# Kernel optimization log

Measured on AMD Instinct MI355X. Metric: run time of the kernel, lower is better.

## Reference

```python
import jax, jax.numpy as jnp
import numpy as np

NODE_DIM, HIDDEN_DIM, OUT_DIM = 64, 128, 64
N_NODES, N_EDGES = 50000, 800000
SLOPE = 0.05


def leaky(x):
    return jnp.where(x >= 0, x, SLOPE * x)


def setup_inputs() -> dict:
    key = jax.random.key(0)
    ks = jax.random.split(key, 8)
    x = jax.random.normal(ks[0], (N_NODES, NODE_DIM), dtype=jnp.float32)
    edge_index = jax.random.randint(ks[1], (2, N_EDGES), 0, N_NODES, dtype=jnp.int64)
    s0 = 1.0 / np.sqrt(NODE_DIM)
    s1 = 1.0 / np.sqrt(HIDDEN_DIM)
    W0 = jax.random.uniform(ks[2], (NODE_DIM, HIDDEN_DIM), jnp.float32, -s0, s0)
    b0 = jax.random.uniform(ks[3], (HIDDEN_DIM,), jnp.float32, -s0, s0)
    W1 = jax.random.uniform(ks[4], (HIDDEN_DIM, HIDDEN_DIM), jnp.float32, -s1, s1)
    b1 = jax.random.uniform(ks[5], (HIDDEN_DIM,), jnp.float32, -s1, s1)
    W2 = jax.random.uniform(ks[6], (HIDDEN_DIM, OUT_DIM), jnp.float32, -s1, s1)
    b2 = jax.random.uniform(ks[7], (OUT_DIM,), jnp.float32, -s1, s1)
    return {"x": x, "edge_index": edge_index, "W0": W0, "b0": b0,
            "W1": W1, "b1": b1, "W2": W2, "b2": b2}


def reference(x, edge_index, W0, b0, W1, b1, W2, b2):
    # gather-sum: [E, node_dim]
    e = x[edge_index[0]] + x[edge_index[1]]
    h = leaky(e @ W0 + b0)          # [E, hidden]
    h = leaky(h @ W1 + b1)          # [E, hidden]
    out = leaky(h @ W2 + b2)        # [E, out]
    return out
```

## Files before the change

kernel.cpp:

```cpp
#include <hip/hip_runtime.h>

typedef _Float16 half8  __attribute__((ext_vector_type(8)));
typedef float    floatx4 __attribute__((ext_vector_type(4)));

#define N_NODES 50000
#define N_EDGES 800000
#define SLOPE 0.05f

#define WS_Z   0ull
#define WS_W1  (WS_Z  + (size_t)N_NODES * 128 * 2)
#define WS_W2  (WS_W1 + 128 * 128 * 2)
#define WS_B0  (WS_W2 + 64 * 128 * 2)
#define WS_B1  (WS_B0 + 128 * 4)
#define WS_B2  (WS_B1 + 128 * 4)

#define W0_STRIDE 72
#define H_STRIDE 136
#define HC_STRIDE 40

__device__ __forceinline__ float leaky(float t) { return t >= 0.f ? t : SLOPE * t; }

__global__ void wprep_kernel(const float* __restrict__ W1, const float* __restrict__ W2,
                             const float* __restrict__ b0, const float* __restrict__ b1,
                             const float* __restrict__ b2, unsigned char* __restrict__ ws) {
    _Float16* wt1 = (_Float16*)(ws + WS_W1);
    _Float16* wt2 = (_Float16*)(ws + WS_W2);
    float* B0 = (float*)(ws + WS_B0);
    float* B1 = (float*)(ws + WS_B1);
    float* B2 = (float*)(ws + WS_B2);
    int t = blockIdx.x * 1024 + threadIdx.x;
    if (t < 16384) {
        int k = t >> 7, n = t & 127;
        wt1[n * 128 + k] = (_Float16)W1[k * 128 + n];
    } else if (t < 24576) {
        int i = t - 16384;
        int k = i >> 6, n = i & 63;
        wt2[n * 128 + k] = (_Float16)W2[k * 64 + n];
    } else if (t < 24576 + 320) {
        int i = t - 24576;
        if (i < 128) B0[i] = b0[i];
        else if (i < 256) B1[i - 128] = b1[i - 128];
        else B2[i - 256] = b2[i - 256];
    }
}

__global__ __launch_bounds__(512, 4) void z_kernel(const float* __restrict__ x,
                                                   const float* __restrict__ W0,
                                                   unsigned char* __restrict__ ws) {
    __shared__ __align__(16) _Float16 w0t[128 * W0_STRIDE];
    __shared__ __align__(16) _Float16 hbuf[8][16 * H_STRIDE];
    _Float16* __restrict__ z = (_Float16*)(ws + WS_Z);

    {
        int t = threadIdx.x;
        int n = t >> 2, k0 = (t & 3) * 16;
        half8 t0, t1;
        #pragma unroll
        for (int j = 0; j < 8; ++j) t0[j] = (_Float16)W0[(k0 + j) * 128 + n];
        #pragma unroll
        for (int j = 0; j < 8; ++j) t1[j] = (_Float16)W0[(k0 + 8 + j) * 128 + n];
        *(half8*)&w0t[n * W0_STRIDE + k0] = t0;
        *(half8*)&w0t[n * W0_STRIDE + k0 + 8] = t1;
    }
    __syncthreads();

    const int wave = threadIdx.x >> 6, lane = threadIdx.x & 63;
    const int cl = lane & 15, q = lane >> 4;
    const int rowbase = blockIdx.x * 128 + wave * 16;
    int row = rowbase + cl; if (row > N_NODES - 1) row = N_NODES - 1;

    half8 a[2];
    #pragma unroll
    for (int ks = 0; ks < 2; ++ks) {
        const floatx4* px = (const floatx4*)(x + (size_t)row * 64 + ks * 32 + q * 8);
        floatx4 u0 = px[0], u1 = px[1];
        #pragma unroll
        for (int j = 0; j < 4; ++j) { a[ks][j] = (_Float16)u0[j]; a[ks][4 + j] = (_Float16)u1[j]; }
    }

    _Float16* hs = &hbuf[wave][0];
    #pragma unroll
    for (int n = 0; n < 8; ++n) {
        floatx4 c = {0.f, 0.f, 0.f, 0.f};
        #pragma unroll
        for (int ks = 0; ks < 2; ++ks) {
            half8 b = *(const half8*)&w0t[(n * 16 + cl) * W0_STRIDE + ks * 32 + q * 8];
            c = __builtin_amdgcn_mfma_f32_16x16x32_f16(a[ks], b, c, 0, 0, 0);
        }
        #pragma unroll
        for (int r = 0; r < 4; ++r)
            hs[(q * 4 + r) * H_STRIDE + n * 16 + cl] = (_Float16)c[r];
    }

    int rl = lane >> 2, ch = lane & 3;
    int grow = rowbase + rl;
    if (grow < N_NODES) {
        #pragma unroll
        for (int i = 0; i < 4; ++i)
            *(half8*)(z + (size_t)grow * 128 + i * 32 + ch * 8) =
                *(const half8*)&hs[rl * H_STRIDE + i * 32 + ch * 8];
    }
}

__global__ __launch_bounds__(512, 4) void edge_kernel(const int* __restrict__ ei,
                                                      const unsigned char* __restrict__ ws,
                                                      float* __restrict__ out) {
    __shared__ __align__(16) _Float16 w1s[128 * H_STRIDE];
    __shared__ __align__(16) _Float16 w2s[64 * H_STRIDE];
    __shared__ __align__(16) _Float16 hc[8][16 * HC_STRIDE];
    __shared__ float b0s[128], b1s[128], b2s[64];

    const _Float16* __restrict__ z    = (const _Float16*)(ws + WS_Z);
    const _Float16* __restrict__ wt1g = (const _Float16*)(ws + WS_W1);
    const _Float16* __restrict__ wt2g = (const _Float16*)(ws + WS_W2);

    {
        int t = threadIdx.x;
        #pragma unroll
        for (int it = 0; it < 4; ++it) {
            int c = t + it * 512;
            int row = c >> 4, cc = c & 15;
            *(half8*)&w1s[row * H_STRIDE + cc * 8] = *(const half8*)&wt1g[row * 128 + cc * 8];
        }
        #pragma unroll
        for (int it = 0; it < 2; ++it) {
            int c = t + it * 512;
            int row = c >> 4, cc = c & 15;
            *(half8*)&w2s[row * H_STRIDE + cc * 8] = *(const half8*)&wt2g[row * 128 + cc * 8];
        }
        if (t < 128) {
            b0s[t] = *(const float*)(ws + WS_B0 + t * 4);
            b1s[t] = *(const float*)(ws + WS_B1 + t * 4);
        } else if (t < 192) {
            b2s[t - 128] = *(const float*)(ws + WS_B2 + (size_t)(t - 128) * 4);
        }
    }
    __syncthreads();

    const int wave = threadIdx.x >> 6, lane = threadIdx.x & 63;
    const int cl = lane & 15, q = lane >> 4;
    const int rowbase = blockIdx.x * 128 + wave * 16;

    const int r = rowbase + cl;
    const int s = ei[r];
    const int d = ei[N_EDGES + r];
    const _Float16* zs = z + (size_t)s * 128;
    const _Float16* zd = z + (size_t)d * 128;

    half8 a1[4];
    #pragma unroll
    for (int ks = 0; ks < 4; ++ks) {
        half8 u = *(const half8*)(zs + ks * 32 + q * 8);
        half8 v = *(const half8*)(zd + ks * 32 + q * 8);
        floatx4 bA = *(const floatx4*)&b0s[ks * 32 + q * 8];
        floatx4 bB = *(const floatx4*)&b0s[ks * 32 + q * 8 + 4];
        #pragma unroll
        for (int j = 0; j < 4; ++j) {
            float t0 = (float)u[j]     + (float)v[j]     + bA[j];
            float t1 = (float)u[4 + j] + (float)v[4 + j] + bB[j];
            a1[ks][j]     = (_Float16)leaky(t0);
            a1[ks][4 + j] = (_Float16)leaky(t1);
        }
    }

    _Float16* hw = &hc[wave][0];
    floatx4 acc2[4];
    #pragma unroll
    for (int n2 = 0; n2 < 4; ++n2) acc2[n2] = (floatx4){0.f, 0.f, 0.f, 0.f};

    #pragma unroll
    for (int ks = 0; ks < 4; ++ks) {
        #pragma unroll
        for (int nn = 0; nn < 2; ++nn) {
            const int n = ks * 2 + nn;
            floatx4 c = {0.f, 0.f, 0.f, 0.f};
            #pragma unroll
            for (int kk = 0; kk < 4; ++kk) {
                half8 b = *(const half8*)&w1s[(n * 16 + cl) * H_STRIDE + kk * 32 + q * 8];
                c = __builtin_amdgcn_mfma_f32_16x16x32_f16(a1[kk], b, c, 0, 0, 0);
            }
            const float bb = b1s[n * 16 + cl];
            #pragma unroll
            for (int rr = 0; rr < 4; ++rr)
                hw[(q * 4 + rr) * HC_STRIDE + nn * 16 + cl] = (_Float16)leaky(c[rr] + bb);
        }
        half8 a2 = *(const half8*)&hw[cl * HC_STRIDE + q * 8];
        #pragma unroll
        for (int n2 = 0; n2 < 4; ++n2) {
            half8 b = *(const half8*)&w2s[(n2 * 16 + cl) * H_STRIDE + ks * 32 + q * 8];
            acc2[n2] = __builtin_amdgcn_mfma_f32_16x16x32_f16(a2, b, acc2[n2], 0, 0, 0);
        }
    }

    #pragma unroll
    for (int n2 = 0; n2 < 4; ++n2) {
        const float bb = b2s[n2 * 16 + cl];
        #pragma unroll
        for (int rr = 0; rr < 4; ++rr)
            out[(size_t)(rowbase + q * 4 + rr) * 64 + n2 * 16 + cl] = leaky(acc2[n2][rr] + bb);
    }
}

extern "C" void kernel_launch(void* const* d_in, const int* in_sizes, int n_in,
                              void* d_out, int out_size, void* d_ws, size_t ws_size,
                              hipStream_t stream) {
    const float* x  = (const float*)d_in[0];
    const int*   ei = (const int*)d_in[1];
    const float* W0 = (const float*)d_in[2];
    const float* b0 = (const float*)d_in[3];
    const float* W1 = (const float*)d_in[4];
    const float* b1 = (const float*)d_in[5];
    const float* W2 = (const float*)d_in[6];
    const float* b2 = (const float*)d_in[7];
    float* out = (float*)d_out;
    unsigned char* ws = (unsigned char*)d_ws;

    wprep_kernel<<<25, 1024, 0, stream>>>(W1, W2, b0, b1, b2, ws);
    z_kernel<<<(N_NODES + 127) / 128, 512, 0, stream>>>(x, W0, ws);
    edge_kernel<<<N_EDGES / 128, 512, 0, stream>>>(ei, ws, out);
}
```

Baseline: 299.0 us.

## Persistent edge kernel with two-group MFMA tiles, index prefetch, merged weight prep

The weight-prep kernel is folded into an extra block of the z kernel, removing one launch. The edge kernel becomes persistent with a 512-block grid, so shared weights are loaded once per block and amortised over many 256-edge tiles. Each wave now handles two 16-edge groups that share B-operand LDS loads, and the next tile's edge indices are prefetched. The second GEMM swaps its operands so the output comes out transposed, which allows vectorised nontemporal float4 stores. In exchange it raises register pressure, and the fixed grid of 512 blocks may underfill the GPU or leave tail imbalance.

```diff
diff --git a/kernel.cpp b/kernel.cpp
--- a/kernel.cpp
+++ b/kernel.cpp
@@ -18,37 +18,43 @@
 #define H_STRIDE 136
 #define HC_STRIDE 40
 
+#define Z_BLOCKS 391
+#define EDGE_TILES (N_EDGES / 256)
+#define EDGE_GRID 512
+
 __device__ __forceinline__ float leaky(float t) { return t >= 0.f ? t : SLOPE * t; }
-
-__global__ void wprep_kernel(const float* __restrict__ W1, const float* __restrict__ W2,
-                             const float* __restrict__ b0, const float* __restrict__ b1,
-                             const float* __restrict__ b2, unsigned char* __restrict__ ws) {
-    _Float16* wt1 = (_Float16*)(ws + WS_W1);
-    _Float16* wt2 = (_Float16*)(ws + WS_W2);
-    float* B0 = (float*)(ws + WS_B0);
-    float* B1 = (float*)(ws + WS_B1);
-    float* B2 = (float*)(ws + WS_B2);
-    int t = blockIdx.x * 1024 + threadIdx.x;
-    if (t < 16384) {
-        int k = t >> 7, n = t & 127;
-        wt1[n * 128 + k] = (_Float16)W1[k * 128 + n];
-    } else if (t < 24576) {
-        int i = t - 16384;
-        int k = i >> 6, n = i & 63;
-        wt2[n * 128 + k] = (_Float16)W2[k * 64 + n];
-    } else if (t < 24576 + 320) {
-        int i = t - 24576;
-        if (i < 128) B0[i] = b0[i];
-        else if (i < 256) B1[i - 128] = b1[i - 128];
-        else B2[i - 256] = b2[i - 256];
-    }
-}
 
 __global__ __launch_bounds__(512, 4) void z_kernel(const float* __restrict__ x,
                                                    const float* __restrict__ W0,
+                                                   const float* __restrict__ W1,
+                                                   const float* __restrict__ W2,
+                                                   const float* __restrict__ b0,
+                                                   const float* __restrict__ b1,
+                                                   const float* __restrict__ b2,
                                                    unsigned char* __restrict__ ws) {
     __shared__ __align__(16) _Float16 w0t[128 * W0_STRIDE];
     __shared__ __align__(16) _Float16 hbuf[8][16 * H_STRIDE];
+
+    if (blockIdx.x == Z_BLOCKS) {
+        _Float16* wt1 = (_Float16*)(ws + WS_W1);
+        _Float16* wt2 = (_Float16*)(ws + WS_W2);
+        float* B0 = (float*)(ws + WS_B0);
+        float* B1 = (float*)(ws + WS_B1);
+        float* B2 = (float*)(ws + WS_B2);
+        for (int t = threadIdx.x; t < 16384; t += 512) {
+            int k = t >> 7, n = t & 127;
+            wt1[n * 128 + k] = (_Float16)W1[k * 128 + n];
+        }
+        for (int t = threadIdx.x; t < 8192; t += 512) {
+            int k = t >> 6, n = t & 63;
+            wt2[n * 128 + k] = (_Float16)W2[k * 64 + n];
+        }
+        if (threadIdx.x < 128) B0[threadIdx.x] = b0[threadIdx.x];
+        else if (threadIdx.x < 256) B1[threadIdx.x - 128] = b1[threadIdx.x - 128];
+        else if (threadIdx.x < 320) B2[threadIdx.x - 256] = b2[threadIdx.x - 256];
+        return;
+    }
+
     _Float16* __restrict__ z = (_Float16*)(ws + WS_Z);
 
     {
@@ -107,12 +113,23 @@
                                                       float* __restrict__ out) {
     __shared__ __align__(16) _Float16 w1s[128 * H_STRIDE];
     __shared__ __align__(16) _Float16 w2s[64 * H_STRIDE];
-    __shared__ __align__(16) _Float16 hc[8][16 * HC_STRIDE];
-    __shared__ float b0s[128], b1s[128], b2s[64];
+    __shared__ __align__(16) _Float16 hc[8][2][16 * HC_STRIDE];
+    __shared__ __align__(16) float b0s[128], b1s[128], b2s[64];
 
     const _Float16* __restrict__ z    = (const _Float16*)(ws + WS_Z);
     const _Float16* __restrict__ wt1g = (const _Float16*)(ws + WS_W1);
     const _Float16* __restrict__ wt2g = (const _Float16*)(ws + WS_W2);
+
+    const int wave = threadIdx.x >> 6, lane = threadIdx.x & 63;
+    const int cl = lane & 15, q = lane >> 4;
+
+    int tile = blockIdx.x;
+    int s0, d0, s1, d1;
+    {
+        const int r0 = tile * 256 + wave * 32 + cl;
+        s0 = ei[r0];      d0 = ei[N_EDGES + r0];
+        s1 = ei[r0 + 16]; d1 = ei[N_EDGES + r0 + 16];
+    }
 
     {
         int t = threadIdx.x;
@@ -137,67 +154,91 @@
     }
     __syncthreads();
 
-    const int wave = threadIdx.x >> 6, lane = threadIdx.x & 63;
-    const int cl = lane & 15, q = lane >> 4;
-    const int rowbase = blockIdx.x * 128 + wave * 16;
-
-    const int r = rowbase + cl;
-    const int s = ei[r];
-    const int d = ei[N_EDGES + r];
-    const _Float16* zs = z + (size_t)s * 128;
-    const _Float16* zd = z + (size_t)d * 128;
-
-    half8 a1[4];
-    #pragma unroll
-    for (int ks = 0; ks < 4; ++ks) {
-        half8 u = *(const half8*)(zs + ks * 32 + q * 8);
-        half8 v = *(const half8*)(zd + ks * 32 + q * 8);
-        floatx4 bA = *(const floatx4*)&b0s[ks * 32 + q * 8];
-        floatx4 bB = *(const floatx4*)&b0s[ks * 32 + q * 8 + 4];
-        #pragma unroll
-        for (int j = 0; j < 4; ++j) {
-            float t0 = (float)u[j]     + (float)v[j]     + bA[j];
-            float t1 = (float)u[4 + j] + (float)v[4 + j] + bB[j];
-            a1[ks][j]     = (_Float16)leaky(t0);
-            a1[ks][4 + j] = (_Float16)leaky(t1);
-        }
-    }
-
-    _Float16* hw = &hc[wave][0];
-    floatx4 acc2[4];
-    #pragma unroll
-    for (int n2 = 0; n2 < 4; ++n2) acc2[n2] = (floatx4){0.f, 0.f, 0.f, 0.f};
-
-    #pragma unroll
-    for (int ks = 0; ks < 4; ++ks) {
-        #pragma unroll
-        for (int nn = 0; nn < 2; ++nn) {
-            const int n = ks * 2 + nn;
-            floatx4 c = {0.f, 0.f, 0.f, 0.f};
-            #pragma unroll
-            for (int kk = 0; kk < 4; ++kk) {
-                half8 b = *(const half8*)&w1s[(n * 16 + cl) * H_STRIDE + kk * 32 + q * 8];
-                c = __builtin_amdgcn_mfma_f32_16x16x32_f16(a1[kk], b, c, 0, 0, 0);
-            }
-            const float bb = b1s[n * 16 + cl];
-            #pragma unroll
-            for (int rr = 0; rr < 4; ++rr)
-                hw[(q * 4 + rr) * HC_STRIDE + nn * 16 + cl] = (_Float16)leaky(c[rr] + bb);
-        }
-        half8 a2 = *(const half8*)&hw[cl * HC_STRIDE + q * 8];
+    for (; tile < EDGE_TILES; tile += EDGE_GRID) {
+        const int base = tile * 256 + wave * 32;
+
+        half8 a1[2][4];
+        #pragma unroll
+        for (int g = 0; g < 2; ++g) {
+            const int ss = g ? s1 : s0, dd = g ? d1 : d0;
+            const _Float16* zs = z + (size_t)ss * 128;
+            const _Float16* zd = z + (size_t)dd * 128;
+            half8 u[4], v[4];
+            #pragma unroll
+            for (int ks = 0; ks < 4; ++ks) {
+                u[ks] = *(const half8*)(zs + ks * 32 + q * 8);
+                v[ks] = *(const half8*)(zd + ks * 32 + q * 8);
+            }
+            #pragma unroll
+            for (int ks = 0; ks < 4; ++ks) {
+                floatx4 bA = *(const floatx4*)&b0s[ks * 32 + q * 8];
+                floatx4 bB = *(const floatx4*)&b0s[ks * 32 + q * 8 + 4];
+                #pragma unroll
+                for (int j = 0; j < 4; ++j) {
+                    float t0 = (float)u[ks][j]     + (float)v[ks][j]     + bA[j];
+                    float t1 = (float)u[ks][4 + j] + (float)v[ks][4 + j] + bB[j];
+                    a1[g][ks][j]     = (_Float16)leaky(t0);
+                    a1[g][ks][4 + j] = (_Float16)leaky(t1);
+                }
+            }
+        }
+
+        {
+            const int nt = tile + EDGE_GRID;
+            if (nt < EDGE_TILES) {
+                const int rn = nt * 256 + wave * 32 + cl;
+                s0 = ei[rn];      d0 = ei[N_EDGES + rn];
+                s1 = ei[rn + 16]; d1 = ei[N_EDGES + rn + 16];
+            }
+        }
+
+        floatx4 acc2[2][4];
+        #pragma unroll
+        for (int g = 0; g < 2; ++g)
+            #pragma unroll
+            for (int n2 = 0; n2 < 4; ++n2) acc2[g][n2] = (floatx4){0.f, 0.f, 0.f, 0.f};
+
+        #pragma unroll
+        for (int ks = 0; ks < 4; ++ks) {
+            #pragma unroll
+            for (int nn = 0; nn < 2; ++nn) {
+                const int n = ks * 2 + nn;
+                floatx4 c0 = {0.f, 0.f, 0.f, 0.f}, c1 = {0.f, 0.f, 0.f, 0.f};
+                #pragma unroll
+                for (int kk = 0; kk < 4; ++kk) {
+                    half8 b = *(const half8*)&w1s[(n * 16 + cl) * H_STRIDE + kk * 32 + q * 8];
+                    c0 = __builtin_amdgcn_mfma_f32_16x16x32_f16(a1[0][kk], b, c0, 0, 0, 0);
+                    c1 = __builtin_amdgcn_mfma_f32_16x16x32_f16(a1[1][kk], b, c1, 0, 0, 0);
+                }
+                const float bb = b1s[n * 16 + cl];
+                #pragma unroll
+                for (int rr = 0; rr < 4; ++rr) {
+                    hc[wave][0][(q * 4 + rr) * HC_STRIDE + nn * 16 + cl] = (_Float16)leaky(c0[rr] + bb);
+                    hc[wave][1][(q * 4 + rr) * HC_STRIDE + nn * 16 + cl] = (_Float16)leaky(c1[rr] + bb);
+                }
+            }
+            half8 a20 = *(const half8*)&hc[wave][0][cl * HC_STRIDE + q * 8];
+            half8 a21 = *(const half8*)&hc[wave][1][cl * HC_STRIDE + q * 8];
+            #pragma unroll
+            for (int n2 = 0; n2 < 4; ++n2) {
+                half8 b = *(const half8*)&w2s[(n2 * 16 + cl) * H_STRIDE + ks * 32 + q * 8];
+                acc2[0][n2] = __builtin_amdgcn_mfma_f32_16x16x32_f16(b, a20, acc2[0][n2], 0, 0, 0);
+                acc2[1][n2] = __builtin_amdgcn_mfma_f32_16x16x32_f16(b, a21, acc2[1][n2], 0, 0, 0);
+            }
+        }
+
         #pragma unroll
         for (int n2 = 0; n2 < 4; ++n2) {
-            half8 b = *(const half8*)&w2s[(n2 * 16 + cl) * H_STRIDE + ks * 32 + q * 8];
-            acc2[n2] = __builtin_amdgcn_mfma_f32_16x16x32_f16(a2, b, acc2[n2], 0, 0, 0);
-        }
-    }
-
-    #pragma unroll
-    for (int n2 = 0; n2 < 4; ++n2) {
-        const float bb = b2s[n2 * 16 + cl];
-        #pragma unroll
-        for (int rr = 0; rr < 4; ++rr)
-            out[(size_t)(rowbase + q * 4 + rr) * 64 + n2 * 16 + cl] = leaky(acc2[n2][rr] + bb);
+            floatx4 bb = *(const floatx4*)&b2s[n2 * 16 + q * 4];
+            #pragma unroll
+            for (int g = 0; g < 2; ++g) {
+                floatx4 o;
+                #pragma unroll
+                for (int rr = 0; rr < 4; ++rr) o[rr] = leaky(acc2[g][n2][rr] + bb[rr]);
+                __builtin_nontemporal_store(o,
+                    (floatx4*)(out + (size_t)(base + g * 16 + cl) * 64 + n2 * 16 + q * 4));
+            }
+        }
     }
 }
 
@@ -215,7 +256,6 @@
     float* out = (float*)d_out;
     unsigned char* ws = (unsigned char*)d_ws;
 
-    wprep_kernel<<<25, 1024, 0, stream>>>(W1, W2, b0, b1, b2, ws);
-    z_kernel<<<(N_NODES + 127) / 128, 512, 0, stream>>>(x, W0, ws);
-    edge_kernel<<<N_EDGES / 128, 512, 0, stream>>>(ei, ws, out);
+    z_kernel<<<Z_BLOCKS + 1, 512, 0, stream>>>(x, W0, W1, W2, b0, b1, b2, ws);
+    edge_kernel<<<EDGE_GRID, 512, 0, stream>>>(ei, ws, out);
 }
```

After: 441.8 us. +47.7%, slower.

## Move W0 matmul into edge kernel, gather fp16 x, double edges per wave

Applied to the files above, without the earlier changes.

Drops the per-node z precompute (x@W0 in fp16, 128 wide). The edge kernel now gathers 64-wide fp16 x rows, adds them, and does the first-layer MFMA itself. This halves gather bytes and removes one kernel launch, at the cost of extra MFMA work per edge. Other changes: each wave handles 32 edges so every weight fragment read from LDS serves two MFMAs, the LDS weight layouts use XOR swizzling instead of padding, gathers are issued before the weight staging, and output stores are vectorised through a transposed final MFMA. Gather-sum rounding shifts slightly because x is rounded to fp16 before the add.

```diff
diff --git a/kernel.cpp b/kernel.cpp
--- a/kernel.cpp
+++ b/kernel.cpp
@@ -7,197 +7,203 @@
 #define N_EDGES 800000
 #define SLOPE 0.05f
 
-#define WS_Z   0ull
-#define WS_W1  (WS_Z  + (size_t)N_NODES * 128 * 2)
+#define WS_XH  0ull
+#define WS_W0  (WS_XH + (size_t)N_NODES * 64 * 2)
+#define WS_W1  (WS_W0 + 128 * 64 * 2)
 #define WS_W2  (WS_W1 + 128 * 128 * 2)
 #define WS_B0  (WS_W2 + 64 * 128 * 2)
 #define WS_B1  (WS_B0 + 128 * 4)
 #define WS_B2  (WS_B1 + 128 * 4)
 
-#define W0_STRIDE 72
-#define H_STRIDE 136
 #define HC_STRIDE 40
+#define XCONV_BLOCKS 782
+#define PREP_BLOCKS (XCONV_BLOCKS + 65)
 
 __device__ __forceinline__ float leaky(float t) { return t >= 0.f ? t : SLOPE * t; }
 
-__global__ void wprep_kernel(const float* __restrict__ W1, const float* __restrict__ W2,
-                             const float* __restrict__ b0, const float* __restrict__ b1,
-                             const float* __restrict__ b2, unsigned char* __restrict__ ws) {
+__global__ void prep_kernel(const float* __restrict__ x,
+                            const float* __restrict__ W0, const float* __restrict__ W1,
+                            const float* __restrict__ W2, const float* __restrict__ b0,
+                            const float* __restrict__ b1, const float* __restrict__ b2,
+                            unsigned char* __restrict__ ws) {
+    const int b = blockIdx.x;
+    if (b < XCONV_BLOCKS) {
+        _Float16* xh = (_Float16*)(ws + WS_XH);
+        const int i = (b * 512 + threadIdx.x) * 8;
+        if (i < N_NODES * 64) {
+            floatx4 u0 = *(const floatx4*)(x + i);
+            floatx4 u1 = *(const floatx4*)(x + i + 4);
+            half8 h;
+            #pragma unroll
+            for (int j = 0; j < 4; ++j) { h[j] = (_Float16)u0[j]; h[4 + j] = (_Float16)u1[j]; }
+            *(half8*)(xh + i) = h;
+        }
+        return;
+    }
+    const int t = (b - XCONV_BLOCKS) * 512 + threadIdx.x;
+    _Float16* w0t = (_Float16*)(ws + WS_W0);
     _Float16* wt1 = (_Float16*)(ws + WS_W1);
     _Float16* wt2 = (_Float16*)(ws + WS_W2);
-    float* B0 = (float*)(ws + WS_B0);
-    float* B1 = (float*)(ws + WS_B1);
-    float* B2 = (float*)(ws + WS_B2);
-    int t = blockIdx.x * 1024 + threadIdx.x;
-    if (t < 16384) {
+    if (t < 8192) {
         int k = t >> 7, n = t & 127;
+        w0t[n * 64 + k] = (_Float16)W0[k * 128 + n];
+    } else if (t < 24576) {
+        int i2 = t - 8192, k = i2 >> 7, n = i2 & 127;
         wt1[n * 128 + k] = (_Float16)W1[k * 128 + n];
-    } else if (t < 24576) {
-        int i = t - 16384;
-        int k = i >> 6, n = i & 63;
+    } else if (t < 32768) {
+        int i2 = t - 24576, k = i2 >> 6, n = i2 & 63;
         wt2[n * 128 + k] = (_Float16)W2[k * 64 + n];
-    } else if (t < 24576 + 320) {
-        int i = t - 24576;
-        if (i < 128) B0[i] = b0[i];
-        else if (i < 256) B1[i - 128] = b1[i - 128];
-        else B2[i - 256] = b2[i - 256];
-    }
-}
-
-__global__ __launch_bounds__(512, 4) void z_kernel(const float* __restrict__ x,
-                                                   const float* __restrict__ W0,
-                                                   unsigned char* __restrict__ ws) {
-    __shared__ __align__(16) _Float16 w0t[128 * W0_STRIDE];
-    __shared__ __align__(16) _Float16 hbuf[8][16 * H_STRIDE];
-    _Float16* __restrict__ z = (_Float16*)(ws + WS_Z);
-
-    {
-        int t = threadIdx.x;
-        int n = t >> 2, k0 = (t & 3) * 16;
-        half8 t0, t1;
-        #pragma unroll
-        for (int j = 0; j < 8; ++j) t0[j] = (_Float16)W0[(k0 + j) * 128 + n];
-        #pragma unroll
-        for (int j = 0; j < 8; ++j) t1[j] = (_Float16)W0[(k0 + 8 + j) * 128 + n];
-        *(half8*)&w0t[n * W0_STRIDE + k0] = t0;
-        *(half8*)&w0t[n * W0_STRIDE + k0 + 8] = t1;
-    }
-    __syncthreads();
-
-    const int wave = threadIdx.x >> 6, lane = threadIdx.x & 63;
-    const int cl = lane & 15, q = lane >> 4;
-    const int rowbase = blockIdx.x * 128 + wave * 16;
-    int row = rowbase + cl; if (row > N_NODES - 1) row = N_NODES - 1;
-
-    half8 a[2];
-    #pragma unroll
-    for (int ks = 0; ks < 2; ++ks) {
-        const floatx4* px = (const floatx4*)(x + (size_t)row * 64 + ks * 32 + q * 8);
-        floatx4 u0 = px[0], u1 = px[1];
-        #pragma unroll
-        for (int j = 0; j < 4; ++j) { a[ks][j] = (_Float16)u0[j]; a[ks][4 + j] = (_Float16)u1[j]; }
-    }
-
-    _Float16* hs = &hbuf[wave][0];
-    #pragma unroll
-    for (int n = 0; n < 8; ++n) {
-        floatx4 c = {0.f, 0.f, 0.f, 0.f};
-        #pragma unroll
-        for (int ks = 0; ks < 2; ++ks) {
-            half8 b = *(const half8*)&w0t[(n * 16 + cl) * W0_STRIDE + ks * 32 + q * 8];
-            c = __builtin_amdgcn_mfma_f32_16x16x32_f16(a[ks], b, c, 0, 0, 0);
-        }
-        #pragma unroll
-        for (int r = 0; r < 4; ++r)
-            hs[(q * 4 + r) * H_STRIDE + n * 16 + cl] = (_Float16)c[r];
-    }
-
-    int rl = lane >> 2, ch = lane & 3;
-    int grow = rowbase + rl;
-    if (grow < N_NODES) {
-        #pragma unroll
-        for (int i = 0; i < 4; ++i)
-            *(half8*)(z + (size_t)grow * 128 + i * 32 + ch * 8) =
-                *(const half8*)&hs[rl * H_STRIDE + i * 32 + ch * 8];
+    } else if (t < 33088) {
+        int i2 = t - 32768;
+        if (i2 < 128) ((float*)(ws + WS_B0))[i2] = b0[i2];
+        else if (i2 < 256) ((float*)(ws + WS_B1))[i2 - 128] = b1[i2 - 128];
+        else ((float*)(ws + WS_B2))[i2 - 256] = b2[i2 - 256];
     }
 }
 
 __global__ __launch_bounds__(512, 4) void edge_kernel(const int* __restrict__ ei,
                                                       const unsigned char* __restrict__ ws,
                                                       float* __restrict__ out) {
-    __shared__ __align__(16) _Float16 w1s[128 * H_STRIDE];
-    __shared__ __align__(16) _Float16 w2s[64 * H_STRIDE];
+    __shared__ __align__(16) _Float16 w0s[128 * 64];
+    __shared__ __align__(16) _Float16 w1s[128 * 128];
+    __shared__ __align__(16) _Float16 w2s[64 * 128];
     __shared__ __align__(16) _Float16 hc[8][16 * HC_STRIDE];
-    __shared__ float b0s[128], b1s[128], b2s[64];
-
-    const _Float16* __restrict__ z    = (const _Float16*)(ws + WS_Z);
-    const _Float16* __restrict__ wt1g = (const _Float16*)(ws + WS_W1);
-    const _Float16* __restrict__ wt2g = (const _Float16*)(ws + WS_W2);
-
-    {
-        int t = threadIdx.x;
-        #pragma unroll
-        for (int it = 0; it < 4; ++it) {
-            int c = t + it * 512;
-            int row = c >> 4, cc = c & 15;
-            *(half8*)&w1s[row * H_STRIDE + cc * 8] = *(const half8*)&wt1g[row * 128 + cc * 8];
-        }
-        #pragma unroll
-        for (int it = 0; it < 2; ++it) {
-            int c = t + it * 512;
-            int row = c >> 4, cc = c & 15;
-            *(half8*)&w2s[row * H_STRIDE + cc * 8] = *(const half8*)&wt2g[row * 128 + cc * 8];
-        }
-        if (t < 128) {
-            b0s[t] = *(const float*)(ws + WS_B0 + t * 4);
-            b1s[t] = *(const float*)(ws + WS_B1 + t * 4);
-        } else if (t < 192) {
-            b2s[t - 128] = *(const float*)(ws + WS_B2 + (size_t)(t - 128) * 4);
-        }
-    }
-    __syncthreads();
+    __shared__ __align__(16) float b0s[128], b1s[128], b2s[64];
+
+    const _Float16* __restrict__ xh  = (const _Float16*)(ws + WS_XH);
+    const _Float16* __restrict__ w0g = (const _Float16*)(ws + WS_W0);
+    const _Float16* __restrict__ w1g = (const _Float16*)(ws + WS_W1);
+    const _Float16* __restrict__ w2g = (const _Float16*)(ws + WS_W2);
 
     const int wave = threadIdx.x >> 6, lane = threadIdx.x & 63;
     const int cl = lane & 15, q = lane >> 4;
-    const int rowbase = blockIdx.x * 128 + wave * 16;
-
-    const int r = rowbase + cl;
-    const int s = ei[r];
-    const int d = ei[N_EDGES + r];
-    const _Float16* zs = z + (size_t)s * 128;
-    const _Float16* zd = z + (size_t)d * 128;
-
-    half8 a1[4];
+    const int base = blockIdx.x * 256 + wave * 32;
+
+    const int r0 = base + cl;
+    const int s0 = ei[r0], d0 = ei[N_EDGES + r0];
+    const int s1 = ei[r0 + 16], d1 = ei[N_EDGES + r0 + 16];
+
+    const _Float16* ps0 = xh + (size_t)s0 * 64 + q * 8;
+    const _Float16* pd0 = xh + (size_t)d0 * 64 + q * 8;
+    const _Float16* ps1 = xh + (size_t)s1 * 64 + q * 8;
+    const _Float16* pd1 = xh + (size_t)d1 * 64 + q * 8;
+    half8 us00 = *(const half8*)(ps0);  half8 us01 = *(const half8*)(ps0 + 32);
+    half8 ud00 = *(const half8*)(pd0);  half8 ud01 = *(const half8*)(pd0 + 32);
+    half8 us10 = *(const half8*)(ps1);  half8 us11 = *(const half8*)(ps1 + 32);
+    half8 ud10 = *(const half8*)(pd1);  half8 ud11 = *(const half8*)(pd1 + 32);
+
+    {
+        const int t = threadIdx.x;
+        #pragma unroll
+        for (int it = 0; it < 4; ++it) {
+            int c = t + it * 512, row = c >> 4, cc = c & 15;
+            int dst = (row * 128 + cc * 8) ^ ((row & 7) << 3);
+            *(half8*)&w1s[dst] = *(const half8*)&w1g[row * 128 + cc * 8];
+        }
+        #pragma unroll
+        for (int it = 0; it < 2; ++it) {
+            int c = t + it * 512, row = c >> 4, cc = c & 15;
+            int dst = (row * 128 + cc * 8) ^ ((row & 7) << 3);
+            *(half8*)&w2s[dst] = *(const half8*)&w2g[row * 128 + cc * 8];
+        }
+        #pragma unroll
+        for (int it = 0; it < 2; ++it) {
+            int c = t + it * 512, row = c >> 3, cc = c & 7;
+            int dst = (row * 64 + cc * 8) ^ ((row & 7) << 3);
+            *(half8*)&w0s[dst] = *(const half8*)&w0g[row * 64 + cc * 8];
+        }
+        if (t < 128) { b0s[t] = *(const float*)(ws + WS_B0 + t * 4);
+                       b1s[t] = *(const float*)(ws + WS_B1 + t * 4); }
+        else if (t < 192) b2s[t - 128] = *(const float*)(ws + WS_B2 + (size_t)(t - 128) * 4);
+    }
+    __syncthreads();
+
+    half8 a0[2][2];
+    a0[0][0] = us00 + ud00;  a0[0][1] = us01 + ud01;
+    a0[1][0] = us10 + ud10;  a0[1][1] = us11 + ud11;
+
+    const int swz = (cl & 7) << 3;
+    _Float16* hw = &hc[wave][0];
+
+    half8 a1[2][4];
+    #pragma unroll
+    for (int kk = 0; kk < 4; ++kk) {
+        const int nA = 2 * kk, nB = 2 * kk + 1;
+        half8 wA0 = *(const half8*)&w0s[((nA * 16 + cl) * 64 + q * 8) ^ swz];
+        half8 wA1 = *(const half8*)&w0s[((nA * 16 + cl) * 64 + 32 + q * 8) ^ swz];
+        half8 wB0 = *(const half8*)&w0s[((nB * 16 + cl) * 64 + q * 8) ^ swz];
+        half8 wB1 = *(const half8*)&w0s[((nB * 16 + cl) * 64 + 32 + q * 8) ^ swz];
+        const float bbA = b0s[nA * 16 + cl], bbB = b0s[nB * 16 + cl];
+        #pragma unroll
+        for (int g = 0; g < 2; ++g) {
+            floatx4 cA = {0.f, 0.f, 0.f, 0.f}, cB = {0.f, 0.f, 0.f, 0.f};
+            cA = __builtin_amdgcn_mfma_f32_16x16x32_f16(a0[g][0], wA0, cA, 0, 0, 0);
+            cA = __builtin_amdgcn_mfma_f32_16x16x32_f16(a0[g][1], wA1, cA, 0, 0, 0);
+            cB = __builtin_amdgcn_mfma_f32_16x16x32_f16(a0[g][0], wB0, cB, 0, 0, 0);
+            cB = __builtin_amdgcn_mfma_f32_16x16x32_f16(a0[g][1], wB1, cB, 0, 0, 0);
+            #pragma unroll
+            for (int rr = 0; rr < 4; ++rr) {
+                hw[(q * 4 + rr) * HC_STRIDE + cl]      = (_Float16)leaky(cA[rr] + bbA);
+                hw[(q * 4 + rr) * HC_STRIDE + 16 + cl] = (_Float16)leaky(cB[rr] + bbB);
+            }
+            a1[g][kk] = *(const half8*)&hw[cl * HC_STRIDE + q * 8];
+        }
+    }
+
+    floatx4 acc2[2][4];
+    #pragma unroll
+    for (int g = 0; g < 2; ++g)
+        #pragma unroll
+        for (int n2 = 0; n2 < 4; ++n2) acc2[g][n2] = (floatx4){0.f, 0.f, 0.f, 0.f};
+
     #pragma unroll
     for (int ks = 0; ks < 4; ++ks) {
-        half8 u = *(const half8*)(zs + ks * 32 + q * 8);
-        half8 v = *(const half8*)(zd + ks * 32 + q * 8);
-        floatx4 bA = *(const floatx4*)&b0s[ks * 32 + q * 8];
-        floatx4 bB = *(const floatx4*)&b0s[ks * 32 + q * 8 + 4];
-        #pragma unroll
-        for (int j = 0; j < 4; ++j) {
-            float t0 = (float)u[j]     + (float)v[j]     + bA[j];
-            float t1 = (float)u[4 + j] + (float)v[4 + j] + bB[j];
-            a1[ks][j]     = (_Float16)leaky(t0);
-            a1[ks][4 + j] = (_Float16)leaky(t1);
-        }
-    }
-
-    _Float16* hw = &hc[wave][0];
-    floatx4 acc2[4];
-    #pragma unroll
-    for (int n2 = 0; n2 < 4; ++n2) acc2[n2] = (floatx4){0.f, 0.f, 0.f, 0.f};
-
-    #pragma unroll
-    for (int ks = 0; ks < 4; ++ks) {
-        #pragma unroll
-        for (int nn = 0; nn < 2; ++nn) {
-            const int n = ks * 2 + nn;
-            floatx4 c = {0.f, 0.f, 0.f, 0.f};
-            #pragma unroll
-            for (int kk = 0; kk < 4; ++kk) {
-                half8 b = *(const half8*)&w1s[(n * 16 + cl) * H_STRIDE + kk * 32 + q * 8];
-                c = __builtin_amdgcn_mfma_f32_16x16x32_f16(a1[kk], b, c, 0, 0, 0);
+        const int nA = 2 * ks, nB = 2 * ks + 1;
+        floatx4 cA0 = {0.f,0.f,0.f,0.f}, cA1 = {0.f,0.f,0.f,0.f};
+        floatx4 cB0 = {0.f,0.f,0.f,0.f}, cB1 = {0.f,0.f,0.f,0.f};
+        #pragma unroll
+        for (int kk = 0; kk < 4; ++kk) {
+            half8 b = *(const half8*)&w1s[((nA * 16 + cl) * 128 + kk * 32 + q * 8) ^ swz];
+            cA0 = __builtin_amdgcn_mfma_f32_16x16x32_f16(a1[0][kk], b, cA0, 0, 0, 0);
+            cA1 = __builtin_amdgcn_mfma_f32_16x16x32_f16(a1[1][kk], b, cA1, 0, 0, 0);
+        }
+        #pragma unroll
+        for (int kk = 0; kk < 4; ++kk) {
+            half8 b = *(const half8*)&w1s[((nB * 16 + cl) * 128 + kk * 32 + q * 8) ^ swz];
+            cB0 = __builtin_amdgcn_mfma_f32_16x16x32_f16(a1[0][kk], b, cB0, 0, 0, 0);
+            cB1 = __builtin_amdgcn_mfma_f32_16x16x32_f16(a1[1][kk], b, cB1, 0, 0, 0);
+        }
+        const float bbA = b1s[nA * 16 + cl], bbB = b1s[nB * 16 + cl];
+        half8 a2[2];
+        #pragma unroll
+        for (int g = 0; g < 2; ++g) {
+            const floatx4 cc0 = g ? cA1 : cA0;
+            const floatx4 cc1 = g ? cB1 : cB0;
+            #pragma unroll
+            for (int rr = 0; rr < 4; ++rr) {
+                hw[(q * 4 + rr) * HC_STRIDE + cl]      = (_Float16)leaky(cc0[rr] + bbA);
+                hw[(q * 4 + rr) * HC_STRIDE + 16 + cl] = (_Float16)leaky(cc1[rr] + bbB);
             }
-            const float bb = b1s[n * 16 + cl];
-            #pragma unroll
-            for (int rr = 0; rr < 4; ++rr)
-                hw[(q * 4 + rr) * HC_STRIDE + nn * 16 + cl] = (_Float16)leaky(c[rr] + bb);
-        }
-        half8 a2 = *(const half8*)&hw[cl * HC_STRIDE + q * 8];
+            a2[g] = *(const half8*)&hw[cl * HC_STRIDE + q * 8];
+        }
         #pragma unroll
         for (int n2 = 0; n2 < 4; ++n2) {
-            half8 b = *(const half8*)&w2s[(n2 * 16 + cl) * H_STRIDE + ks * 32 + q * 8];
-            acc2[n2] = __builtin_amdgcn_mfma_f32_16x16x32_f16(a2, b, acc2[n2], 0, 0, 0);
+            half8 b = *(const half8*)&w2s[((n2 * 16 + cl) * 128 + ks * 32 + q * 8) ^ swz];
+            acc2[0][n2] = __builtin_amdgcn_mfma_f32_16x16x32_f16(b, a2[0], acc2[0][n2], 0, 0, 0);
+            acc2[1][n2] = __builtin_amdgcn_mfma_f32_16x16x32_f16(b, a2[1], acc2[1][n2], 0, 0, 0);
         }
     }
 
     #pragma unroll
     for (int n2 = 0; n2 < 4; ++n2) {
-        const float bb = b2s[n2 * 16 + cl];
-        #pragma unroll
-        for (int rr = 0; rr < 4; ++rr)
-            out[(size_t)(rowbase + q * 4 + rr) * 64 + n2 * 16 + cl] = leaky(acc2[n2][rr] + bb);
+        floatx4 bb = *(const floatx4*)&b2s[n2 * 16 + q * 4];
+        #pragma unroll
+        for (int g = 0; g < 2; ++g) {
+            floatx4 o;
+            #pragma unroll
+            for (int rr = 0; rr < 4; ++rr) o[rr] = leaky(acc2[g][n2][rr] + bb[rr]);
+            *(floatx4*)(out + (size_t)(base + g * 16 + cl) * 64 + n2 * 16 + q * 4) = o;
+        }
     }
 }
 
@@ -215,7 +221,6 @@
     float* out = (float*)d_out;
     unsigned char* ws = (unsigned char*)d_ws;
 
-    wprep_kernel<<<25, 1024, 0, stream>>>(W1, W2, b0, b1, b2, ws);
-    z_kernel<<<(N_NODES + 127) / 128, 512, 0, stream>>>(x, W0, ws);
-    edge_kernel<<<N_EDGES / 128, 512, 0, stream>>>(ei, ws, out);
+    prep_kernel<<<PREP_BLOCKS, 512, 0, stream>>>(x, W0, W1, W2, b0, b1, b2, ws);
+    edge_kernel<<<N_EDGES / 256, 512, 0, stream>>>(ei, ws, out);
 }
```

Result: faster. 276.1 us (-7.7%).
